# Performance work log

Hardware: AMD Instinct MI355X
Metric: run time of the kernel (lower is better)

Reference implementation:

```python
import jax, jax.numpy as jnp
import numpy as np

B, T, N, C = 32, 12, 2048, 1
D, K, H = 10, 2, 32


def setup_inputs() -> dict:
    key = jax.random.key(0)
    ks = jax.random.split(key, 8)
    s = 0.1  # small init scale for params
    return {
        "source": jax.random.normal(ks[0], (B, T, N, C), jnp.float32),
        "node_emb": jax.random.normal(ks[1], (N, D), jnp.float32),
        "gate_W": jax.random.normal(ks[2], (D, K, C + H, 2 * H), jnp.float32) * s,
        "gate_b": jax.random.normal(ks[3], (D, 2 * H), jnp.float32) * s,
        "upd_W": jax.random.normal(ks[4], (D, K, C + H, H), jnp.float32) * s,
        "upd_b": jax.random.normal(ks[5], (D, H), jnp.float32) * s,
        "conv_W": jax.random.normal(ks[6], (T * C, 1, 1, H), jnp.float32) * s,
        "conv_b": jax.random.normal(ks[7], (T * C,), jnp.float32) * s,
    }


def reference(source, node_emb, gate_W, gate_b, upd_W, upd_b, conv_W, conv_b):
    b, t, n, c = source.shape
    h = upd_W.shape[-1]
    k = gate_W.shape[1]
    dt = source.dtype
    E = node_emb

    # Adaptive adjacency from node embeddings (time-invariant -> hoist out of scan)
    A = jax.nn.softmax(jax.nn.relu(E @ E.T), axis=1)  # [N,N]
    sup = [jnp.eye(n, dtype=dt), A]
    for i in range(2, k):
        sup.append(2.0 * (A @ sup[-1]) - sup[-2])  # Chebyshev recursion
    S = jnp.stack(sup, 0)  # [K,N,N]

    # Node-specific weights/biases from embedding pools (also time-invariant)
    Wg = jnp.einsum('nd,dkio->nkio', E, gate_W)
    bg = E @ gate_b
    Wu = jnp.einsum('nd,dkio->nkio', E, upd_W)
    bu = E @ upd_b

    def gconv(x, W, bias):  # x: [B,N,Cin] -> [B,N,Cout]
        xg = jnp.einsum('knm,bmc->bnkc', S, x)
        return jnp.einsum('bnki,nkio->bno', xg, W) + bias

    def step(state, xt):  # GRU-style AGCRN cell
        xs = jnp.concatenate([xt, state], axis=-1)
        zr = jax.nn.sigmoid(gconv(xs, Wg, bg))
        z, r = jnp.split(zr, 2, axis=-1)
        hc = jnp.tanh(gconv(jnp.concatenate([xt, z * state], axis=-1), Wu, bu))
        hnew = r * state + (1.0 - r) * hc
        return hnew, None

    h0 = jnp.zeros((b, n, h), dtype=dt)
    h_last, _ = jax.lax.scan(step, h0, jnp.swapaxes(source, 0, 1))  # carry = last state

    # end_conv: Conv2d(1, T*C, kernel=(1,H)) on [B,1,N,H] == matmul over H
    out = jnp.einsum('bnh,oh->bon', h_last, conv_W[:, 0, 0, :]) + conv_b[None, :, None]
    out = out.reshape(b, t, c, n).transpose(0, 2, 3, 1)  # [B, C, N, T]
    return out
```

## Files before the change

### kernel.cpp

```cpp
#include <hip/hip_runtime.h>
#include <hip/hip_bf16.h>
#include <math.h>


#define NNODE 2048
#define NB 32
#define NT 12
#define NH 32
#define ND 10
#define NCOL 1024
#define NCX 384
#define KPAD 96
#define GPAD 104
#define WPAD 98

#define ASCALE 256.0f
#define AINV 0.00390625f

#define KSPLIT 4
#define KCHUNK 512
#define Y1S ((size_t)NNODE * NCOL)
#define AXPS ((size_t)NNODE * NCX)

typedef _Float16 half8 __attribute__((ext_vector_type(8)));
typedef float floatx4 __attribute__((ext_vector_type(4)));

#define AS1 __attribute__((address_space(1)))
#define AS3 __attribute__((address_space(3)))
__device__ __forceinline__ void gload16(const _Float16* g, _Float16* l) {
    __builtin_amdgcn_global_load_lds((const AS1 unsigned int*)(g),
                                     (AS3 unsigned int*)(l), 16, 0, 0);
}

constexpr size_t OFF_AH  = 0;
constexpr size_t OFF_WGT = OFF_AH + 2097152u;
constexpr size_t OFF_WUT = OFF_WGT + 6291456u;
constexpr size_t OFF_BG  = OFF_WUT + 3145728u;
constexpr size_t OFF_BU  = OFF_BG + 131072u;
constexpr size_t OFF_XT  = OFF_BU + 65536u;
constexpr size_t OFF_X2T = OFF_XT + 1048576u;
constexpr size_t OFF_SXT = OFF_X2T + 1048576u;
constexpr size_t OFF_HS  = OFF_SXT + 393216u;
constexpr size_t OFF_Y   = OFF_HS + 2097152u;
constexpr size_t OFF_AXP = OFF_Y + 4194304u;
constexpr size_t OFF_R   = OFF_AXP + 1572864u;
constexpr size_t OFF_ZH  = OFF_R + 1048576u;

__global__ __launch_bounds__(256) void adj_kernel(const float* __restrict__ E,
                                                  _Float16* __restrict__ Ah) {
    __shared__ float En[ND];
    __shared__ float red[256];
    const int n = blockIdx.x;
    const int t = threadIdx.x;
    if (t < ND) En[t] = E[n * ND + t];
    __syncthreads();
    float v[8];
    float mx = 0.f;
#pragma unroll
    for (int i = 0; i < 8; ++i) {
        const int m = t + i * 256;
        float acc = 0.f;
#pragma unroll
        for (int d = 0; d < ND; ++d) acc += En[d] * E[m * ND + d];
        acc = fmaxf(acc, 0.f);
        v[i] = acc;
        mx = fmaxf(mx, acc);
    }
    red[t] = mx;
    __syncthreads();
    for (int s = 128; s > 0; s >>= 1) {
        if (t < s) red[t] = fmaxf(red[t], red[t + s]);
        __syncthreads();
    }
    mx = red[0];
    __syncthreads();
    float sum = 0.f;
#pragma unroll
    for (int i = 0; i < 8; ++i) {
        v[i] = expf(v[i] - mx);
        sum += v[i];
    }
    red[t] = sum;
    __syncthreads();
    for (int s = 128; s > 0; s >>= 1) {
        if (t < s) red[t] += red[t + s];
        __syncthreads();
    }
    const float inv = ASCALE / red[0];
#pragma unroll
    for (int i = 0; i < 8; ++i)
        Ah[(size_t)n * NNODE + t + i * 256] = (_Float16)(v[i] * inv);
}

__global__ __launch_bounds__(256) void wg_kernel(const float* __restrict__ E,
                                                 const float* __restrict__ gW,
                                                 _Float16* __restrict__ Wgt) {
    __shared__ float Es[ND];
    __shared__ _Float16 Wl[64 * WPAD];
    const int n = blockIdx.x, t = threadIdx.x;
    if (t < ND) Es[t] = E[n * ND + t];
    for (int i = t; i < 64 * WPAD / 2; i += 256) ((unsigned*)Wl)[i] = 0u;
    __syncthreads();
    for (int rem = t; rem < 4224; rem += 256) {
        float acc = 0.f;
#pragma unroll
        for (int d = 0; d < ND; ++d) acc += Es[d] * gW[d * 4224 + rem];
        const int kk = rem / 2112, r2 = rem % 2112;
        const int i = r2 >> 6, o = r2 & 63;
        Wl[o * WPAD + kk * 33 + i] = (_Float16)acc;
    }
    __syncthreads();
    const unsigned* wl = (const unsigned*)Wl;
    unsigned* dst = (unsigned*)(Wgt + (size_t)n * 6144);
    for (int idx = t; idx < 64 * 48; idx += 256) {
        const int o = idx / 48, j = idx % 48;
        dst[idx] = wl[o * (WPAD / 2) + j];
    }
}

__global__ __launch_bounds__(256) void wu_kernel(const float* __restrict__ E,
                                                 const float* __restrict__ uW,
                                                 _Float16* __restrict__ Wut) {
    __shared__ float Es[ND];
    __shared__ _Float16 Wl[32 * WPAD];
    const int n = blockIdx.x, t = threadIdx.x;
    if (t < ND) Es[t] = E[n * ND + t];
    for (int i = t; i < 32 * WPAD / 2; i += 256) ((unsigned*)Wl)[i] = 0u;
    __syncthreads();
    for (int rem = t; rem < 2112; rem += 256) {
        float acc = 0.f;
#pragma unroll
        for (int d = 0; d < ND; ++d) acc += Es[d] * uW[d * 2112 + rem];
        const int kk = rem / 1056, r2 = rem % 1056;
        const int i = r2 >> 5, o = r2 & 31;
        Wl[o * WPAD + kk * 33 + i] = (_Float16)acc;
    }
    __syncthreads();
    const unsigned* wl = (const unsigned*)Wl;
    unsigned* dst = (unsigned*)(Wut + (size_t)n * 3072);
    for (int idx = t; idx < 32 * 48; idx += 256) {
        const int o = idx / 48, j = idx % 48;
        dst[idx] = wl[o * (WPAD / 2) + j];
    }
}

__global__ __launch_bounds__(256) void bias_kernel(const float* __restrict__ E,
                                                   const float* __restrict__ gb,
                                                   const float* __restrict__ ub,
                                                   float* __restrict__ bg,
                                                   float* __restrict__ bu) {
    const int idx = blockIdx.x * 256 + threadIdx.x;
    if (idx < NNODE * 64) {
        const int n = idx >> 6, o = idx & 63;
        float acc = 0.f;
#pragma unroll
        for (int d = 0; d < ND; ++d) acc += E[n * ND + d] * gb[d * 64 + o];
        bg[idx] = acc;
    } else if (idx < NNODE * 64 + NNODE * 32) {
        const int j = idx - NNODE * 64;
        const int n = j >> 5, o = j & 31;
        float acc = 0.f;
#pragma unroll
        for (int d = 0; d < ND; ++d) acc += E[n * ND + d] * ub[d * 32 + o];
        bu[j] = acc;
    }
}

__global__ __launch_bounds__(256) void setup_kernel(const float* __restrict__ src,
                                                    _Float16* __restrict__ XT,
                                                    _Float16* __restrict__ X2T,
                                                    _Float16* __restrict__ SXT,
                                                    float* __restrict__ Hs) {
    const int idx = blockIdx.x * 256 + threadIdx.x;
    XT[idx] = (_Float16)0.f;
    X2T[idx] = (_Float16)0.f;
    Hs[idx] = 0.f;
    if (idx < NCX * NNODE) {
        const int col = idx / NNODE, n = idx % NNODE;
        const int tt = col >> 5, b = col & 31;
        SXT[idx] = (_Float16)src[((size_t)b * NT + tt) * NNODE + n];
    }
}

__global__ __launch_bounds__(256) void mm_kernel(const _Float16* __restrict__ Ah,
                                                 const _Float16* __restrict__ XT,
                                                 _Float16* __restrict__ Y, int nct) {
    __shared__ _Float16 As[128 * 32];
    __shared__ _Float16 Bs[128 * 32];
    const int t = threadIdx.x;
    const int bid = blockIdx.x;
    const int xcd = bid & 7;
    const int kz = xcd >> 1;
    const int s = (bid >> 3) * 2 + (xcd & 1);
    const int m0 = (s & 15) * 128;
    const int c0 = (s >> 4) * 128;
    const int ncols = nct << 7;
    _Float16* __restrict__ Yp = Y + (size_t)kz * NNODE * ncols;
    const int lane = t & 63;
    const int w = t >> 6;
    const int wm = (w & 1) * 64;
    const int wn = (w >> 1) * 64;
    const int lm = lane & 15;
    const int q = lane >> 4;

    const int srow = w * 32 + (lane >> 2);
    const int sq = (lane & 3) ^ ((lane >> 3) & 3);
    const _Float16* gA = Ah + (size_t)(m0 + srow) * NNODE + kz * KCHUNK + sq * 8;
    const _Float16* gB = XT + (size_t)(c0 + srow) * NNODE + kz * KCHUNK + sq * 8;
    _Float16* lA = As + w * 1024;
    _Float16* lB = Bs + w * 1024;

    const int fp = (q ^ ((lm >> 1) & 3)) * 8;

    floatx4 acc[4][4] = {};

    for (int kt = 0; kt < KCHUNK; kt += 32) {
        gload16(gA, lA);
        gload16(gA + 16 * NNODE, lA + 512);
        gload16(gB, lB);
        gload16(gB + 16 * NNODE, lB + 512);
        gA += 32;
        gB += 32;
        __syncthreads();
        half8 af[4], bf[4];
#pragma unroll
        for (int mt = 0; mt < 4; ++mt)
            af[mt] = *(const half8*)&As[(wm + mt * 16 + lm) * 32 + fp];
#pragma unroll
        for (int nt = 0; nt < 4; ++nt)
            bf[nt] = *(const half8*)&Bs[(wn + nt * 16 + lm) * 32 + fp];
#pragma unroll
        for (int mt = 0; mt < 4; ++mt)
#pragma unroll
            for (int nt = 0; nt < 4; ++nt)
                acc[mt][nt] = __builtin_amdgcn_mfma_f32_16x16x32_f16(
                    af[mt], bf[nt], acc[mt][nt], 0, 0, 0);
        __syncthreads();
    }
#pragma unroll
    for (int mt = 0; mt < 4; ++mt) {
#pragma unroll
        for (int nt = 0; nt < 4; ++nt) {
            const int row = m0 + wm + mt * 16 + q * 4;
            const int col = c0 + wn + nt * 16 + lm;
#pragma unroll
            for (int r = 0; r < 4; ++r)
                Yp[(size_t)(row + r) * ncols + col] = (_Float16)(acc[mt][nt][r] * AINV);
        }
    }
}

__global__ __launch_bounds__(256) void gate_kernel(const float* __restrict__ src, int tcur,
                                                   const _Float16* __restrict__ Y,
                                                   const _Float16* __restrict__ AXP,
                                                   const _Float16* __restrict__ Wgt,
                                                   const float* __restrict__ bg,
                                                   const float* __restrict__ Hs,
                                                   _Float16* __restrict__ X2T,
                                                   _Float16* __restrict__ zh,
                                                   _Float16* __restrict__ rbuf) {
    __shared__ _Float16 catL[4][32][GPAD];
    const int t = threadIdx.x;
    const int n0 = blockIdx.x * 4;
    {
        const int pair = t >> 1, which = t & 1;
        const int nd = pair >> 5, b = pair & 31;
        const int n1 = n0 + nd;
        if (which == 0) {
            catL[nd][b][0] = (_Float16)src[((size_t)b * NT + tcur) * NNODE + n1];
            const float* hp = Hs + (size_t)n1 * 1024 + b * 32;
#pragma unroll
            for (int i = 0; i < 32; ++i) catL[nd][b][1 + i] = (_Float16)hp[i];
#pragma unroll
            for (int i = 66; i < KPAD; i += 2) *(unsigned*)&catL[nd][b][i] = 0u;
        } else {
            const _Float16* ax = AXP + (size_t)n1 * NCX + tcur * 32 + b;
            catL[nd][b][33] = (_Float16)((float)ax[0] + (float)ax[AXPS] +
                                         (float)ax[2 * AXPS] + (float)ax[3 * AXPS]);
            const _Float16* yp = Y + (size_t)n1 * NCOL + b * 32;
#pragma unroll
            for (int i = 0; i < 32; ++i) {
                const float sv = (float)yp[i] + (float)yp[Y1S + i] +
                                 (float)yp[2 * Y1S + i] + (float)yp[3 * Y1S + i];
                catL[nd][b][34 + i] = (_Float16)sv;
            }
        }
    }
    __syncthreads();
    const int w = t >> 6, lane = t & 63, lm = lane & 15, q = lane >> 4;
    const int n = n0 + w;
    const _Float16* Wn = Wgt + (size_t)n * 6144;
    floatx4 acc[2][4] = {};
#pragma unroll
    for (int kt = 0; kt < 3; ++kt) {
        half8 af[2], bf[4];
#pragma unroll
        for (int mt = 0; mt < 2; ++mt)
            af[mt] = *(const half8*)&catL[w][mt * 16 + lm][kt * 32 + q * 8];
#pragma unroll
        for (int nt = 0; nt < 4; ++nt)
            bf[nt] = *(const half8*)(Wn + (nt * 16 + lm) * KPAD + kt * 32 + q * 8);
#pragma unroll
        for (int mt = 0; mt < 2; ++mt)
#pragma unroll
            for (int nt = 0; nt < 4; ++nt)
                acc[mt][nt] = __builtin_amdgcn_mfma_f32_16x16x32_f16(
                    af[mt], bf[nt], acc[mt][nt], 0, 0, 0);
    }
#pragma unroll
    for (int nt = 0; nt < 4; ++nt) {
        const int o = nt * 16 + lm;
        const float bias = bg[n * 64 + o];
#pragma unroll
        for (int mt = 0; mt < 2; ++mt) {
#pragma unroll
            for (int r = 0; r < 4; ++r) {
                const int b = mt * 16 + q * 4 + r;
                const float s = 1.f / (1.f + expf(-(acc[mt][nt][r] + bias)));
                if (o < 32) {
                    const float hold = Hs[(size_t)n * 1024 + b * 32 + o];
                    const _Float16 zv = (_Float16)(s * hold);
                    zh[(size_t)n * 1024 + b * 32 + o] = zv;
                    X2T[(size_t)(b * 32 + o) * NNODE + n] = zv;
                } else {
                    rbuf[(size_t)n * 1024 + b * 32 + (o - 32)] = (_Float16)s;
                }
            }
        }
    }
}

__global__ __launch_bounds__(256) void upd_kernel(const float* __restrict__ src, int tcur,
                                                  const _Float16* __restrict__ Y,
                                                  const _Float16* __restrict__ AXP,
                                                  const _Float16* __restrict__ Wut,
                                                  const float* __restrict__ bu,
                                                  const _Float16* __restrict__ zh,
                                                  const _Float16* __restrict__ rbuf,
                                                  float* __restrict__ Hs,
                                                  _Float16* __restrict__ XT) {
    __shared__ _Float16 catL[4][32][GPAD];
    const int t = threadIdx.x;
    const int n0 = blockIdx.x * 4;
    {
        const int pair = t >> 1, which = t & 1;
        const int nd = pair >> 5, b = pair & 31;
        const int n1 = n0 + nd;
        if (which == 0) {
            catL[nd][b][0] = (_Float16)src[((size_t)b * NT + tcur) * NNODE + n1];
            const _Float16* zp = zh + (size_t)n1 * 1024 + b * 32;
#pragma unroll
            for (int i = 0; i < 32; ++i) catL[nd][b][1 + i] = zp[i];
#pragma unroll
            for (int i = 66; i < KPAD; i += 2) *(unsigned*)&catL[nd][b][i] = 0u;
        } else {
            const _Float16* ax = AXP + (size_t)n1 * NCX + tcur * 32 + b;
            catL[nd][b][33] = (_Float16)((float)ax[0] + (float)ax[AXPS] +
                                         (float)ax[2 * AXPS] + (float)ax[3 * AXPS]);
            const _Float16* yp = Y + (size_t)n1 * NCOL + b * 32;
#pragma unroll
            for (int i = 0; i < 32; ++i) {
                const float sv = (float)yp[i] + (float)yp[Y1S + i] +
                                 (float)yp[2 * Y1S + i] + (float)yp[3 * Y1S + i];
                catL[nd][b][34 + i] = (_Float16)sv;
            }
        }
    }
    __syncthreads();
    const int w = t >> 6, lane = t & 63, lm = lane & 15, q = lane >> 4;
    const int n = n0 + w;
    const _Float16* Wn = Wut + (size_t)n * 3072;
    floatx4 acc[2][2] = {};
#pragma unroll
    for (int kt = 0; kt < 3; ++kt) {
        half8 af[2], bf[2];
#pragma unroll
        for (int mt = 0; mt < 2; ++mt)
            af[mt] = *(const half8*)&catL[w][mt * 16 + lm][kt * 32 + q * 8];
#pragma unroll
        for (int nt = 0; nt < 2; ++nt)
            bf[nt] = *(const half8*)(Wn + (nt * 16 + lm) * KPAD + kt * 32 + q * 8);
#pragma unroll
        for (int mt = 0; mt < 2; ++mt)
#pragma unroll
            for (int nt = 0; nt < 2; ++nt)
                acc[mt][nt] = __builtin_amdgcn_mfma_f32_16x16x32_f16(
                    af[mt], bf[nt], acc[mt][nt], 0, 0, 0);
    }
#pragma unroll
    for (int nt = 0; nt < 2; ++nt) {
        const int o = nt * 16 + lm;
        const float bias = bu[n * 32 + o];
#pragma unroll
        for (int mt = 0; mt < 2; ++mt) {
#pragma unroll
            for (int r = 0; r < 4; ++r) {
                const int b = mt * 16 + q * 4 + r;
                const float hc = tanhf(acc[mt][nt][r] + bias);
                const float rr = (float)rbuf[(size_t)n * 1024 + b * 32 + o];
                const size_t hidx = (size_t)n * 1024 + b * 32 + o;
                const float hnew = rr * Hs[hidx] + (1.f - rr) * hc;
                Hs[hidx] = hnew;
                XT[(size_t)(b * 32 + o) * NNODE + n] = (_Float16)hnew;
            }
        }
    }
}

__global__ __launch_bounds__(256) void out_kernel(const float* __restrict__ Hs,
                                                  const float* __restrict__ cw,
                                                  const float* __restrict__ cb,
                                                  float* __restrict__ out) {
    __shared__ float h[NB * NH];
    __shared__ float cws[NT * NH];
    __shared__ float cbs[NT];
    const int n = blockIdx.x;
    const int t = threadIdx.x;
    for (int i = t; i < NT * NH; i += 256) cws[i] = cw[i];
    if (t < NT) cbs[t] = cb[t];
    for (int i = t; i < NB * NH; i += 256) h[i] = Hs[(size_t)n * 1024 + i];
    __syncthreads();
    for (int p = t; p < NB * NT; p += 256) {
        const int b = p / NT, tt = p % NT;
        float acc = cbs[tt];
#pragma unroll
        for (int j = 0; j < NH; ++j) acc += h[b * NH + j] * cws[tt * NH + j];
        out[(size_t)b * NNODE * NT + (size_t)n * NT + tt] = acc;
    }
}

extern "C" void kernel_launch(void* const* d_in, const int* in_sizes, int n_in,
                              void* d_out, int out_size, void* d_ws, size_t ws_size,
                              hipStream_t stream) {
    const float* src  = (const float*)d_in[0];
    const float* E    = (const float*)d_in[1];
    const float* gW   = (const float*)d_in[2];
    const float* gb   = (const float*)d_in[3];
    const float* uW   = (const float*)d_in[4];
    const float* ub   = (const float*)d_in[5];
    const float* cw   = (const float*)d_in[6];
    const float* cb   = (const float*)d_in[7];
    float* out = (float*)d_out;

    float* ws = (float*)d_ws;
    _Float16* Ah  = (_Float16*)(ws + OFF_AH);
    _Float16* Wgt = (_Float16*)(ws + OFF_WGT);
    _Float16* Wut = (_Float16*)(ws + OFF_WUT);
    float* bg  = ws + OFF_BG;
    float* bu  = ws + OFF_BU;
    _Float16* XT  = (_Float16*)(ws + OFF_XT);
    _Float16* X2T = (_Float16*)(ws + OFF_X2T);
    _Float16* SXT = (_Float16*)(ws + OFF_SXT);
    float* Hs  = ws + OFF_HS;
    _Float16* Y   = (_Float16*)(ws + OFF_Y);
    _Float16* AXP = (_Float16*)(ws + OFF_AXP);
    _Float16* rb  = (_Float16*)(ws + OFF_R);
    _Float16* zh  = (_Float16*)(ws + OFF_ZH);

    adj_kernel<<<NNODE, 256, 0, stream>>>(E, Ah);
    wg_kernel<<<NNODE, 256, 0, stream>>>(E, gW, Wgt);
    wu_kernel<<<NNODE, 256, 0, stream>>>(E, uW, Wut);
    bias_kernel<<<(NNODE * 96 + 255) / 256, 256, 0, stream>>>(E, gb, ub, bg, bu);
    setup_kernel<<<NNODE * NCOL / 256, 256, 0, stream>>>(src, XT, X2T, SXT, Hs);

    mm_kernel<<<64 * 3, 256, 0, stream>>>(Ah, SXT, AXP, 3);

    for (int t = 0; t < NT; ++t) {
        mm_kernel<<<64 * 8, 256, 0, stream>>>(Ah, XT, Y, 8);
        gate_kernel<<<NNODE / 4, 256, 0, stream>>>(src, t, Y, AXP, Wgt, bg, Hs, X2T, zh, rb);
        mm_kernel<<<64 * 8, 256, 0, stream>>>(Ah, X2T, Y, 8);
        upd_kernel<<<NNODE / 4, 256, 0, stream>>>(src, t, Y, AXP, Wut, bu, zh, rb, Hs, XT);
    }
    out_kernel<<<NNODE, 256, 0, stream>>>(Hs, cw, cb, out);
}
```

Before: 1.167 ms.

## Fuse recurrent loop into persistent megakernel with software grid barriers

Replaces the 48 per-step launches (matmul, gate, matmul, update) plus the setup and output kernels with one persistent kernel. Phases are separated by an atomic-counter grid barrier. This removes launch overhead and the gaps between kernels, and shares LDS between the matmul tiles and the gate/update staging. It relies on every block being co-resident; if occupancy is misjudged the barrier can deadlock. Serialized barriers and fewer blocks than before (256/512) may also reduce parallelism in some phases.

```diff
diff --git a/kernel.cpp b/kernel.cpp
--- a/kernel.cpp
+++ b/kernel.cpp
@@ -1,7 +1,6 @@
 #include <hip/hip_runtime.h>
 #include <hip/hip_bf16.h>
 #include <math.h>
-
 
 #define NNODE 2048
 #define NB 32
@@ -17,7 +16,6 @@
 #define ASCALE 256.0f
 #define AINV 0.00390625f
 
-#define KSPLIT 4
 #define KCHUNK 512
 #define Y1S ((size_t)NNODE * NCOL)
 #define AXPS ((size_t)NNODE * NCX)
@@ -45,6 +43,28 @@
 constexpr size_t OFF_AXP = OFF_Y + 4194304u;
 constexpr size_t OFF_R   = OFF_AXP + 1572864u;
 constexpr size_t OFF_ZH  = OFF_R + 1048576u;
+constexpr size_t OFF_BAR = OFF_ZH + 1048576u;
+
+__device__ __forceinline__ void gbar(unsigned* bar, int nb) {
+    __syncthreads();
+    if (threadIdx.x == 0) {
+        unsigned g = __hip_atomic_load(bar + 1, __ATOMIC_RELAXED, __HIP_MEMORY_SCOPE_AGENT);
+        unsigned a = __hip_atomic_fetch_add(bar, 1u, __ATOMIC_ACQ_REL, __HIP_MEMORY_SCOPE_AGENT);
+        if (a == (unsigned)nb - 1u) {
+            __hip_atomic_store(bar, 0u, __ATOMIC_RELAXED, __HIP_MEMORY_SCOPE_AGENT);
+            __hip_atomic_store(bar + 1, g + 1u, __ATOMIC_RELEASE, __HIP_MEMORY_SCOPE_AGENT);
+        } else {
+            while (__hip_atomic_load(bar + 1, __ATOMIC_ACQUIRE, __HIP_MEMORY_SCOPE_AGENT) == g)
+                __builtin_amdgcn_s_sleep(2);
+        }
+    }
+    __syncthreads();
+}
+
+__global__ void bar_init(unsigned* bar) {
+    __hip_atomic_store(bar, 0u, __ATOMIC_RELEASE, __HIP_MEMORY_SCOPE_AGENT);
+    __hip_atomic_store(bar + 1, 0u, __ATOMIC_RELEASE, __HIP_MEMORY_SCOPE_AGENT);
+}
 
 __global__ __launch_bounds__(256) void adj_kernel(const float* __restrict__ E,
                                                   _Float16* __restrict__ Ah) {
@@ -166,32 +186,13 @@
     }
 }
 
-__global__ __launch_bounds__(256) void setup_kernel(const float* __restrict__ src,
-                                                    _Float16* __restrict__ XT,
-                                                    _Float16* __restrict__ X2T,
-                                                    _Float16* __restrict__ SXT,
-                                                    float* __restrict__ Hs) {
-    const int idx = blockIdx.x * 256 + threadIdx.x;
-    XT[idx] = (_Float16)0.f;
-    X2T[idx] = (_Float16)0.f;
-    Hs[idx] = 0.f;
-    if (idx < NCX * NNODE) {
-        const int col = idx / NNODE, n = idx % NNODE;
-        const int tt = col >> 5, b = col & 31;
-        SXT[idx] = (_Float16)src[((size_t)b * NT + tt) * NNODE + n];
-    }
-}
-
-__global__ __launch_bounds__(256) void mm_kernel(const _Float16* __restrict__ Ah,
-                                                 const _Float16* __restrict__ XT,
-                                                 _Float16* __restrict__ Y, int nct) {
-    __shared__ _Float16 As[128 * 32];
-    __shared__ _Float16 Bs[128 * 32];
-    const int t = threadIdx.x;
-    const int bid = blockIdx.x;
-    const int xcd = bid & 7;
+__device__ __forceinline__ void mm_tile(const _Float16* __restrict__ Ah,
+                                        const _Float16* __restrict__ XT,
+                                        _Float16* __restrict__ Y, int nct,
+                                        int task, int t, _Float16* As, _Float16* Bs) {
+    const int xcd = task & 7;
     const int kz = xcd >> 1;
-    const int s = (bid >> 3) * 2 + (xcd & 1);
+    const int s = (task >> 3) * 2 + (xcd & 1);
     const int m0 = (s & 15) * 128;
     const int c0 = (s >> 4) * 128;
     const int ncols = nct << 7;
@@ -209,7 +210,6 @@
     const _Float16* gB = XT + (size_t)(c0 + srow) * NNODE + kz * KCHUNK + sq * 8;
     _Float16* lA = As + w * 1024;
     _Float16* lB = Bs + w * 1024;
-
     const int fp = (q ^ ((lm >> 1) & 3)) * 8;
 
     floatx4 acc[4][4] = {};
@@ -250,181 +250,199 @@
     }
 }
 
-__global__ __launch_bounds__(256) void gate_kernel(const float* __restrict__ src, int tcur,
-                                                   const _Float16* __restrict__ Y,
-                                                   const _Float16* __restrict__ AXP,
-                                                   const _Float16* __restrict__ Wgt,
-                                                   const float* __restrict__ bg,
-                                                   const float* __restrict__ Hs,
-                                                   _Float16* __restrict__ X2T,
-                                                   _Float16* __restrict__ zh,
-                                                   _Float16* __restrict__ rbuf) {
-    __shared__ _Float16 catL[4][32][GPAD];
+#define CAT(nd, b, i) cat[((nd) * 32 + (b)) * GPAD + (i)]
+
+__global__ __launch_bounds__(256, 2) void mega_kernel(
+    const float* __restrict__ src, const _Float16* __restrict__ Ah,
+    const _Float16* __restrict__ Wgt, const _Float16* __restrict__ Wut,
+    const float* __restrict__ bg, const float* __restrict__ bu,
+    const float* __restrict__ cw, const float* __restrict__ cb,
+    _Float16* __restrict__ XT, _Float16* __restrict__ X2T,
+    _Float16* __restrict__ SXT, float* __restrict__ Hs,
+    _Float16* __restrict__ Y, _Float16* __restrict__ AXP,
+    _Float16* __restrict__ rbuf, _Float16* __restrict__ zh,
+    float* __restrict__ out, unsigned* bar, int nb) {
+    __shared__ __align__(16) _Float16 smem[4 * 32 * GPAD];
+    _Float16* As = smem;
+    _Float16* Bs = smem + 4096;
+    _Float16* cat = smem;
     const int t = threadIdx.x;
-    const int n0 = blockIdx.x * 4;
+    const int bid = blockIdx.x;
+    const int w = t >> 6, lane = t & 63, lm = lane & 15, q = lane >> 4;
+
     {
-        const int pair = t >> 1, which = t & 1;
-        const int nd = pair >> 5, b = pair & 31;
-        const int n1 = n0 + nd;
-        if (which == 0) {
-            catL[nd][b][0] = (_Float16)src[((size_t)b * NT + tcur) * NNODE + n1];
-            const float* hp = Hs + (size_t)n1 * 1024 + b * 32;
-#pragma unroll
-            for (int i = 0; i < 32; ++i) catL[nd][b][1 + i] = (_Float16)hp[i];
-#pragma unroll
-            for (int i = 66; i < KPAD; i += 2) *(unsigned*)&catL[nd][b][i] = 0u;
-        } else {
-            const _Float16* ax = AXP + (size_t)n1 * NCX + tcur * 32 + b;
-            catL[nd][b][33] = (_Float16)((float)ax[0] + (float)ax[AXPS] +
-                                         (float)ax[2 * AXPS] + (float)ax[3 * AXPS]);
-            const _Float16* yp = Y + (size_t)n1 * NCOL + b * 32;
-#pragma unroll
-            for (int i = 0; i < 32; ++i) {
-                const float sv = (float)yp[i] + (float)yp[Y1S + i] +
-                                 (float)yp[2 * Y1S + i] + (float)yp[3 * Y1S + i];
-                catL[nd][b][34 + i] = (_Float16)sv;
-            }
+        unsigned* p = (unsigned*)XT;
+        for (int idx = bid * 256 + t; idx < 1048576; idx += nb * 256) p[idx] = 0u;
+        unsigned* ph = (unsigned*)Hs;
+        for (int idx = bid * 256 + t; idx < 2097152; idx += nb * 256) ph[idx] = 0u;
+        for (int idx = bid * 256 + t; idx < NCX * NNODE; idx += nb * 256) {
+            const int col = idx >> 11, n = idx & 2047;
+            const int tt = col >> 5, b = col & 31;
+            SXT[idx] = (_Float16)src[((size_t)b * NT + tt) * NNODE + n];
         }
     }
-    __syncthreads();
-    const int w = t >> 6, lane = t & 63, lm = lane & 15, q = lane >> 4;
-    const int n = n0 + w;
-    const _Float16* Wn = Wgt + (size_t)n * 6144;
-    floatx4 acc[2][4] = {};
-#pragma unroll
-    for (int kt = 0; kt < 3; ++kt) {
-        half8 af[2], bf[4];
-#pragma unroll
-        for (int mt = 0; mt < 2; ++mt)
-            af[mt] = *(const half8*)&catL[w][mt * 16 + lm][kt * 32 + q * 8];
-#pragma unroll
-        for (int nt = 0; nt < 4; ++nt)
-            bf[nt] = *(const half8*)(Wn + (nt * 16 + lm) * KPAD + kt * 32 + q * 8);
-#pragma unroll
-        for (int mt = 0; mt < 2; ++mt)
-#pragma unroll
-            for (int nt = 0; nt < 4; ++nt)
-                acc[mt][nt] = __builtin_amdgcn_mfma_f32_16x16x32_f16(
-                    af[mt], bf[nt], acc[mt][nt], 0, 0, 0);
-    }
-#pragma unroll
-    for (int nt = 0; nt < 4; ++nt) {
-        const int o = nt * 16 + lm;
-        const float bias = bg[n * 64 + o];
-#pragma unroll
-        for (int mt = 0; mt < 2; ++mt) {
-#pragma unroll
-            for (int r = 0; r < 4; ++r) {
-                const int b = mt * 16 + q * 4 + r;
-                const float s = 1.f / (1.f + expf(-(acc[mt][nt][r] + bias)));
-                if (o < 32) {
-                    const float hold = Hs[(size_t)n * 1024 + b * 32 + o];
-                    const _Float16 zv = (_Float16)(s * hold);
-                    zh[(size_t)n * 1024 + b * 32 + o] = zv;
-                    X2T[(size_t)(b * 32 + o) * NNODE + n] = zv;
+    gbar(bar, nb);
+
+    for (int task = bid; task < 192; task += nb)
+        mm_tile(Ah, SXT, AXP, 3, task, t, As, Bs);
+    gbar(bar, nb);
+
+    for (int step = 0; step < NT; ++step) {
+        for (int task = bid; task < 512; task += nb)
+            mm_tile(Ah, XT, Y, 8, task, t, As, Bs);
+        gbar(bar, nb);
+
+        for (int g = bid; g < 512; g += nb) {
+            const int n0 = g * 4;
+            {
+                const int pair = t >> 1, which = t & 1;
+                const int nd = pair >> 5, b = pair & 31;
+                const int n1 = n0 + nd;
+                if (which == 0) {
+                    CAT(nd, b, 0) = (_Float16)src[((size_t)b * NT + step) * NNODE + n1];
+                    const float* hp = Hs + (size_t)n1 * 1024 + b * 32;
+#pragma unroll
+                    for (int i = 0; i < 32; ++i) CAT(nd, b, 1 + i) = (_Float16)hp[i];
+#pragma unroll
+                    for (int i = 66; i < KPAD; i += 2) *(unsigned*)&CAT(nd, b, i) = 0u;
                 } else {
-                    rbuf[(size_t)n * 1024 + b * 32 + (o - 32)] = (_Float16)s;
+                    const _Float16* ax = AXP + (size_t)n1 * NCX + step * 32 + b;
+                    CAT(nd, b, 33) = (_Float16)((float)ax[0] + (float)ax[AXPS] +
+                                                (float)ax[2 * AXPS] + (float)ax[3 * AXPS]);
+                    const _Float16* yp = Y + (size_t)n1 * NCOL + b * 32;
+#pragma unroll
+                    for (int i = 0; i < 32; ++i) {
+                        const float sv = (float)yp[i] + (float)yp[Y1S + i] +
+                                         (float)yp[2 * Y1S + i] + (float)yp[3 * Y1S + i];
+                        CAT(nd, b, 34 + i) = (_Float16)sv;
+                    }
                 }
             }
+            __syncthreads();
+            const int n = n0 + w;
+            const _Float16* Wn = Wgt + (size_t)n * 6144;
+            floatx4 acc[2][4] = {};
+#pragma unroll
+            for (int kt = 0; kt < 3; ++kt) {
+                half8 af[2], bf[4];
+#pragma unroll
+                for (int mt = 0; mt < 2; ++mt)
+                    af[mt] = *(const half8*)&CAT(w, mt * 16 + lm, kt * 32 + q * 8);
+#pragma unroll
+                for (int nt = 0; nt < 4; ++nt)
+                    bf[nt] = *(const half8*)(Wn + (nt * 16 + lm) * KPAD + kt * 32 + q * 8);
+#pragma unroll
+                for (int mt = 0; mt < 2; ++mt)
+#pragma unroll
+                    for (int nt = 0; nt < 4; ++nt)
+                        acc[mt][nt] = __builtin_amdgcn_mfma_f32_16x16x32_f16(
+                            af[mt], bf[nt], acc[mt][nt], 0, 0, 0);
+            }
+#pragma unroll
+            for (int nt = 0; nt < 4; ++nt) {
+                const int o = nt * 16 + lm;
+                const float bias = bg[n * 64 + o];
+#pragma unroll
+                for (int mt = 0; mt < 2; ++mt) {
+#pragma unroll
+                    for (int r = 0; r < 4; ++r) {
+                        const int b = mt * 16 + q * 4 + r;
+                        const float s = 1.f / (1.f + expf(-(acc[mt][nt][r] + bias)));
+                        if (o < 32) {
+                            const float hold = Hs[(size_t)n * 1024 + b * 32 + o];
+                            const _Float16 zv = (_Float16)(s * hold);
+                            zh[(size_t)n * 1024 + b * 32 + o] = zv;
+                            X2T[(size_t)(b * 32 + o) * NNODE + n] = zv;
+                        } else {
+                            rbuf[(size_t)n * 1024 + b * 32 + (o - 32)] = (_Float16)s;
+                        }
+                    }
+                }
+            }
+            __syncthreads();
         }
-    }
-}
-
-__global__ __launch_bounds__(256) void upd_kernel(const float* __restrict__ src, int tcur,
-                                                  const _Float16* __restrict__ Y,
-                                                  const _Float16* __restrict__ AXP,
-                                                  const _Float16* __restrict__ Wut,
-                                                  const float* __restrict__ bu,
-                                                  const _Float16* __restrict__ zh,
-                                                  const _Float16* __restrict__ rbuf,
-                                                  float* __restrict__ Hs,
-                                                  _Float16* __restrict__ XT) {
-    __shared__ _Float16 catL[4][32][GPAD];
-    const int t = threadIdx.x;
-    const int n0 = blockIdx.x * 4;
-    {
-        const int pair = t >> 1, which = t & 1;
-        const int nd = pair >> 5, b = pair & 31;
-        const int n1 = n0 + nd;
-        if (which == 0) {
-            catL[nd][b][0] = (_Float16)src[((size_t)b * NT + tcur) * NNODE + n1];
-            const _Float16* zp = zh + (size_t)n1 * 1024 + b * 32;
-#pragma unroll
-            for (int i = 0; i < 32; ++i) catL[nd][b][1 + i] = zp[i];
-#pragma unroll
-            for (int i = 66; i < KPAD; i += 2) *(unsigned*)&catL[nd][b][i] = 0u;
-        } else {
-            const _Float16* ax = AXP + (size_t)n1 * NCX + tcur * 32 + b;
-            catL[nd][b][33] = (_Float16)((float)ax[0] + (float)ax[AXPS] +
-                                         (float)ax[2 * AXPS] + (float)ax[3 * AXPS]);
-            const _Float16* yp = Y + (size_t)n1 * NCOL + b * 32;
-#pragma unroll
-            for (int i = 0; i < 32; ++i) {
-                const float sv = (float)yp[i] + (float)yp[Y1S + i] +
-                                 (float)yp[2 * Y1S + i] + (float)yp[3 * Y1S + i];
-                catL[nd][b][34 + i] = (_Float16)sv;
-            }
+        gbar(bar, nb);
+
+        for (int task = bid; task < 512; task += nb)
+            mm_tile(Ah, X2T, Y, 8, task, t, As, Bs);
+        gbar(bar, nb);
+
+        for (int g = bid; g < 512; g += nb) {
+            const int n0 = g * 4;
+            {
+                const int pair = t >> 1, which = t & 1;
+                const int nd = pair >> 5, b = pair & 31;
+                const int n1 = n0 + nd;
+                if (which == 0) {
+                    CAT(nd, b, 0) = (_Float16)src[((size_t)b * NT + step) * NNODE + n1];
+                    const _Float16* zp = zh + (size_t)n1 * 1024 + b * 32;
+#pragma unroll
+                    for (int i = 0; i < 32; ++i) CAT(nd, b, 1 + i) = zp[i];
+#pragma unroll
+                    for (int i = 66; i < KPAD; i += 2) *(unsigned*)&CAT(nd, b, i) = 0u;
+                } else {
+                    const _Float16* ax = AXP + (size_t)n1 * NCX + step * 32 + b;
+                    CAT(nd, b, 33) = (_Float16)((float)ax[0] + (float)ax[AXPS] +
+                                                (float)ax[2 * AXPS] + (float)ax[3 * AXPS]);
+                    const _Float16* yp = Y + (size_t)n1 * NCOL + b * 32;
+#pragma unroll
+                    for (int i = 0; i < 32; ++i) {
+                        const float sv = (float)yp[i] + (float)yp[Y1S + i] +
+                                         (float)yp[2 * Y1S + i] + (float)yp[3 * Y1S + i];
+                        CAT(nd, b, 34 + i) = (_Float16)sv;
+                    }
+                }
+            }
+            __syncthreads();
+            const int n = n0 + w;
+            const _Float16* Wn = Wut + (size_t)n * 3072;
+            floatx4 acc[2][2] = {};
+#pragma unroll
+            for (int kt = 0; kt < 3; ++kt) {
+                half8 af[2], bf[2];
+#pragma unroll
+                for (int mt = 0; mt < 2; ++mt)
+                    af[mt] = *(const half8*)&CAT(w, mt * 16 + lm, kt * 32 + q * 8);
+#pragma unroll
+                for (int nt = 0; nt < 2; ++nt)
+                    bf[nt] = *(const half8*)(Wn + (nt * 16 + lm) * KPAD + kt * 32 + q * 8);
+#pragma unroll
+                for (int mt = 0; mt < 2; ++mt)
+#pragma unroll
+                    for (int nt = 0; nt < 2; ++nt)
+                        acc[mt][nt] = __builtin_amdgcn_mfma_f32_16x16x32_f16(
+                            af[mt], bf[nt], acc[mt][nt], 0, 0, 0);
+            }
+#pragma unroll
+            for (int nt = 0; nt < 2; ++nt) {
+                const int o = nt * 16 + lm;
+                const float bias = bu[n * 32 + o];
+#pragma unroll
+                for (int mt = 0; mt < 2; ++mt) {
+#pragma unroll
+                    for (int r = 0; r < 4; ++r) {
+                        const int b = mt * 16 + q * 4 + r;
+                        const float hc = tanhf(acc[mt][nt][r] + bias);
+                        const float rr = (float)rbuf[(size_t)n * 1024 + b * 32 + o];
+                        const size_t hidx = (size_t)n * 1024 + b * 32 + o;
+                        const float hnew = rr * Hs[hidx] + (1.f - rr) * hc;
+                        Hs[hidx] = hnew;
+                        XT[(size_t)(b * 32 + o) * NNODE + n] = (_Float16)hnew;
+                    }
+                }
+            }
+            __syncthreads();
         }
-    }
-    __syncthreads();
-    const int w = t >> 6, lane = t & 63, lm = lane & 15, q = lane >> 4;
-    const int n = n0 + w;
-    const _Float16* Wn = Wut + (size_t)n * 3072;
-    floatx4 acc[2][2] = {};
-#pragma unroll
-    for (int kt = 0; kt < 3; ++kt) {
-        half8 af[2], bf[2];
-#pragma unroll
-        for (int mt = 0; mt < 2; ++mt)
-            af[mt] = *(const half8*)&catL[w][mt * 16 + lm][kt * 32 + q * 8];
-#pragma unroll
-        for (int nt = 0; nt < 2; ++nt)
-            bf[nt] = *(const half8*)(Wn + (nt * 16 + lm) * KPAD + kt * 32 + q * 8);
-#pragma unroll
-        for (int mt = 0; mt < 2; ++mt)
-#pragma unroll
-            for (int nt = 0; nt < 2; ++nt)
-                acc[mt][nt] = __builtin_amdgcn_mfma_f32_16x16x32_f16(
-                    af[mt], bf[nt], acc[mt][nt], 0, 0, 0);
-    }
-#pragma unroll
-    for (int nt = 0; nt < 2; ++nt) {
-        const int o = nt * 16 + lm;
-        const float bias = bu[n * 32 + o];
-#pragma unroll
-        for (int mt = 0; mt < 2; ++mt) {
-#pragma unroll
-            for (int r = 0; r < 4; ++r) {
-                const int b = mt * 16 + q * 4 + r;
-                const float hc = tanhf(acc[mt][nt][r] + bias);
-                const float rr = (float)rbuf[(size_t)n * 1024 + b * 32 + o];
-                const size_t hidx = (size_t)n * 1024 + b * 32 + o;
-                const float hnew = rr * Hs[hidx] + (1.f - rr) * hc;
-                Hs[hidx] = hnew;
-                XT[(size_t)(b * 32 + o) * NNODE + n] = (_Float16)hnew;
-            }
-        }
-    }
-}
-
-__global__ __launch_bounds__(256) void out_kernel(const float* __restrict__ Hs,
-                                                  const float* __restrict__ cw,
-                                                  const float* __restrict__ cb,
-                                                  float* __restrict__ out) {
-    __shared__ float h[NB * NH];
-    __shared__ float cws[NT * NH];
-    __shared__ float cbs[NT];
-    const int n = blockIdx.x;
-    const int t = threadIdx.x;
-    for (int i = t; i < NT * NH; i += 256) cws[i] = cw[i];
-    if (t < NT) cbs[t] = cb[t];
-    for (int i = t; i < NB * NH; i += 256) h[i] = Hs[(size_t)n * 1024 + i];
-    __syncthreads();
-    for (int p = t; p < NB * NT; p += 256) {
-        const int b = p / NT, tt = p % NT;
-        float acc = cbs[tt];
-#pragma unroll
-        for (int j = 0; j < NH; ++j) acc += h[b * NH + j] * cws[tt * NH + j];
+        gbar(bar, nb);
+    }
+
+    for (int p = bid * 256 + t; p < NNODE * NB * NT; p += nb * 256) {
+        const int n = p / 384, rem = p % 384;
+        const int b = rem / NT, tt = rem % NT;
+        float acc = cb[tt];
+        const float* hp = Hs + (size_t)n * 1024 + b * 32;
+#pragma unroll
+        for (int j = 0; j < NH; ++j) acc += hp[j] * cw[tt * 32 + j];
         out[(size_t)b * NNODE * NT + (size_t)n * NT + tt] = acc;
     }
 }
@@ -456,20 +474,19 @@
     _Float16* AXP = (_Float16*)(ws + OFF_AXP);
     _Float16* rb  = (_Float16*)(ws + OFF_R);
     _Float16* zh  = (_Float16*)(ws + OFF_ZH);
+    unsigned* bar = (unsigned*)(ws + OFF_BAR);
 
     adj_kernel<<<NNODE, 256, 0, stream>>>(E, Ah);
     wg_kernel<<<NNODE, 256, 0, stream>>>(E, gW, Wgt);
     wu_kernel<<<NNODE, 256, 0, stream>>>(E, uW, Wut);
     bias_kernel<<<(NNODE * 96 + 255) / 256, 256, 0, stream>>>(E, gb, ub, bg, bu);
-    setup_kernel<<<NNODE * NCOL / 256, 256, 0, stream>>>(src, XT, X2T, SXT, Hs);
-
-    mm_kernel<<<64 * 3, 256, 0, stream>>>(Ah, SXT, AXP, 3);
-
-    for (int t = 0; t < NT; ++t) {
-        mm_kernel<<<64 * 8, 256, 0, stream>>>(Ah, XT, Y, 8);
-        gate_kernel<<<NNODE / 4, 256, 0, stream>>>(src, t, Y, AXP, Wgt, bg, Hs, X2T, zh, rb);
-        mm_kernel<<<64 * 8, 256, 0, stream>>>(Ah, X2T, Y, 8);
-        upd_kernel<<<NNODE / 4, 256, 0, stream>>>(src, t, Y, AXP, Wut, bu, zh, rb, Hs, XT);
-    }
-    out_kernel<<<NNODE, 256, 0, stream>>>(Hs, cw, cb, out);
-}
+    bar_init<<<1, 1, 0, stream>>>(bar);
+
+    int occ = 0;
+    hipOccupancyMaxActiveBlocksPerMultiprocessor(&occ, mega_kernel, 256, 0);
+    const int nb = (occ >= 2) ? 512 : 256;
+
+    mega_kernel<<<nb, 256, 0, stream>>>(src, Ah, Wgt, Wut, bg, bu, cw, cb,
+                                        XT, X2T, SXT, Hs, Y, AXP, rb, zh,
+                                        out, bar, nb);
+}
```

Result: slower. 3.411 ms (+192.4%).

## Fuse propagation matmul with gate/update cells using per-row-chunk atomic counters

Applied to the files above, without the earlier changes.

Each step's mm_kernel is merged into the gate and update kernels, giving one 512-block kernel per half-step. Each block first computes one matmul tile and signals an atomic counter for its row chunk. It then spin-waits until all 32 tiles covering its node rows are done before running the GRU cell. This removes half the per-step launches and the full-grid barriers between matmul and cell, and shares LDS between the two phases. It relies on all 512 blocks being co-resident (two per CU under the launch bounds) to avoid deadlock, and it adds spin-wait and fence overhead.

```diff
diff --git a/kernel.cpp b/kernel.cpp
--- a/kernel.cpp
+++ b/kernel.cpp
@@ -1,7 +1,6 @@
 #include <hip/hip_runtime.h>
 #include <hip/hip_bf16.h>
 #include <math.h>
-
 
 #define NNODE 2048
 #define NB 32
@@ -17,7 +16,6 @@
 #define ASCALE 256.0f
 #define AINV 0.00390625f
 
-#define KSPLIT 4
 #define KCHUNK 512
 #define Y1S ((size_t)NNODE * NCOL)
 #define AXPS ((size_t)NNODE * NCX)
@@ -45,6 +43,7 @@
 constexpr size_t OFF_AXP = OFF_Y + 4194304u;
 constexpr size_t OFF_R   = OFF_AXP + 1572864u;
 constexpr size_t OFF_ZH  = OFF_R + 1048576u;
+constexpr size_t OFF_CNT = OFF_ZH + 1048576u;
 
 __global__ __launch_bounds__(256) void adj_kernel(const float* __restrict__ E,
                                                   _Float16* __restrict__ Ah) {
@@ -170,28 +169,27 @@
                                                     _Float16* __restrict__ XT,
                                                     _Float16* __restrict__ X2T,
                                                     _Float16* __restrict__ SXT,
-                                                    float* __restrict__ Hs) {
+                                                    float* __restrict__ Hs,
+                                                    unsigned* __restrict__ cnt) {
     const int idx = blockIdx.x * 256 + threadIdx.x;
     XT[idx] = (_Float16)0.f;
     X2T[idx] = (_Float16)0.f;
     Hs[idx] = 0.f;
     if (idx < NCX * NNODE) {
-        const int col = idx / NNODE, n = idx % NNODE;
+        const int col = idx >> 11, n = idx & 2047;
         const int tt = col >> 5, b = col & 31;
         SXT[idx] = (_Float16)src[((size_t)b * NT + tt) * NNODE + n];
     }
-}
-
-__global__ __launch_bounds__(256) void mm_kernel(const _Float16* __restrict__ Ah,
-                                                 const _Float16* __restrict__ XT,
-                                                 _Float16* __restrict__ Y, int nct) {
-    __shared__ _Float16 As[128 * 32];
-    __shared__ _Float16 Bs[128 * 32];
-    const int t = threadIdx.x;
-    const int bid = blockIdx.x;
-    const int xcd = bid & 7;
+    if (idx < 384) cnt[idx] = 0u;
+}
+
+__device__ __forceinline__ void mm_tile(const _Float16* __restrict__ Ah,
+                                        const _Float16* __restrict__ XT,
+                                        _Float16* __restrict__ Y, int nct,
+                                        int task, int t, _Float16* As, _Float16* Bs) {
+    const int xcd = task & 7;
     const int kz = xcd >> 1;
-    const int s = (bid >> 3) * 2 + (xcd & 1);
+    const int s = (task >> 3) * 2 + (xcd & 1);
     const int m0 = (s & 15) * 128;
     const int c0 = (s >> 4) * 128;
     const int ncols = nct << 7;
@@ -209,7 +207,6 @@
     const _Float16* gB = XT + (size_t)(c0 + srow) * NNODE + kz * KCHUNK + sq * 8;
     _Float16* lA = As + w * 1024;
     _Float16* lB = Bs + w * 1024;
-
     const int fp = (q ^ ((lm >> 1) & 3)) * 8;
 
     floatx4 acc[4][4] = {};
@@ -250,44 +247,69 @@
     }
 }
 
-__global__ __launch_bounds__(256) void gate_kernel(const float* __restrict__ src, int tcur,
-                                                   const _Float16* __restrict__ Y,
-                                                   const _Float16* __restrict__ AXP,
-                                                   const _Float16* __restrict__ Wgt,
-                                                   const float* __restrict__ bg,
-                                                   const float* __restrict__ Hs,
-                                                   _Float16* __restrict__ X2T,
-                                                   _Float16* __restrict__ zh,
-                                                   _Float16* __restrict__ rbuf) {
-    __shared__ _Float16 catL[4][32][GPAD];
-    const int t = threadIdx.x;
-    const int n0 = blockIdx.x * 4;
+__device__ __forceinline__ void signal_wait(unsigned* cnt, int bid, int t) {
+    __threadfence();
+    __syncthreads();
+    if (t == 0) {
+        const int sp = (bid >> 3) * 2 + (bid & 1);
+        __hip_atomic_fetch_add(&cnt[sp & 15], 1u, __ATOMIC_RELEASE,
+                               __HIP_MEMORY_SCOPE_AGENT);
+        const int rc = bid >> 5;
+        unsigned v;
+        do {
+            v = __hip_atomic_load(&cnt[rc], __ATOMIC_RELAXED, __HIP_MEMORY_SCOPE_AGENT);
+            if (v < 32u) __builtin_amdgcn_s_sleep(1);
+        } while (v < 32u);
+        (void)__hip_atomic_load(&cnt[rc], __ATOMIC_ACQUIRE, __HIP_MEMORY_SCOPE_AGENT);
+    }
+    __syncthreads();
+}
+
+#define CAT(nd, b, i) cat[((nd) * 32 + (b)) * GPAD + (i)]
+
+__global__ __launch_bounds__(256, 2) void mmgate_kernel(
+    const float* __restrict__ src, int tcur, const _Float16* __restrict__ Ah,
+    const _Float16* __restrict__ XT, _Float16* __restrict__ Y,
+    const _Float16* __restrict__ AXP, const _Float16* __restrict__ Wgt,
+    const float* __restrict__ bg, const float* __restrict__ Hs,
+    _Float16* __restrict__ X2T, _Float16* __restrict__ zh,
+    _Float16* __restrict__ rbuf, unsigned* __restrict__ cnt) {
+    __shared__ __align__(16) _Float16 smem[4 * 32 * GPAD];
+    _Float16* As = smem;
+    _Float16* Bs = smem + 4096;
+    _Float16* cat = smem;
+    const int t = threadIdx.x, bid = blockIdx.x;
+    const int w = t >> 6, lane = t & 63, lm = lane & 15, q = lane >> 4;
+
+    mm_tile(Ah, XT, Y, 8, bid, t, As, Bs);
+    signal_wait(cnt, bid, t);
+
+    const int n0 = bid * 4;
     {
         const int pair = t >> 1, which = t & 1;
         const int nd = pair >> 5, b = pair & 31;
         const int n1 = n0 + nd;
         if (which == 0) {
-            catL[nd][b][0] = (_Float16)src[((size_t)b * NT + tcur) * NNODE + n1];
+            CAT(nd, b, 0) = (_Float16)src[((size_t)b * NT + tcur) * NNODE + n1];
             const float* hp = Hs + (size_t)n1 * 1024 + b * 32;
 #pragma unroll
-            for (int i = 0; i < 32; ++i) catL[nd][b][1 + i] = (_Float16)hp[i];
-#pragma unroll
-            for (int i = 66; i < KPAD; i += 2) *(unsigned*)&catL[nd][b][i] = 0u;
+            for (int i = 0; i < 32; ++i) CAT(nd, b, 1 + i) = (_Float16)hp[i];
+#pragma unroll
+            for (int i = 66; i < KPAD; i += 2) *(unsigned*)&CAT(nd, b, i) = 0u;
         } else {
             const _Float16* ax = AXP + (size_t)n1 * NCX + tcur * 32 + b;
-            catL[nd][b][33] = (_Float16)((float)ax[0] + (float)ax[AXPS] +
-                                         (float)ax[2 * AXPS] + (float)ax[3 * AXPS]);
+            CAT(nd, b, 33) = (_Float16)((float)ax[0] + (float)ax[AXPS] +
+                                        (float)ax[2 * AXPS] + (float)ax[3 * AXPS]);
             const _Float16* yp = Y + (size_t)n1 * NCOL + b * 32;
 #pragma unroll
             for (int i = 0; i < 32; ++i) {
                 const float sv = (float)yp[i] + (float)yp[Y1S + i] +
                                  (float)yp[2 * Y1S + i] + (float)yp[3 * Y1S + i];
-                catL[nd][b][34 + i] = (_Float16)sv;
+                CAT(nd, b, 34 + i) = (_Float16)sv;
             }
         }
     }
     __syncthreads();
-    const int w = t >> 6, lane = t & 63, lm = lane & 15, q = lane >> 4;
     const int n = n0 + w;
     const _Float16* Wn = Wgt + (size_t)n * 6144;
     floatx4 acc[2][4] = {};
@@ -296,7 +318,7 @@
         half8 af[2], bf[4];
 #pragma unroll
         for (int mt = 0; mt < 2; ++mt)
-            af[mt] = *(const half8*)&catL[w][mt * 16 + lm][kt * 32 + q * 8];
+            af[mt] = *(const half8*)&CAT(w, mt * 16 + lm, kt * 32 + q * 8);
 #pragma unroll
         for (int nt = 0; nt < 4; ++nt)
             bf[nt] = *(const half8*)(Wn + (nt * 16 + lm) * KPAD + kt * 32 + q * 8);
@@ -330,44 +352,49 @@
     }
 }
 
-__global__ __launch_bounds__(256) void upd_kernel(const float* __restrict__ src, int tcur,
-                                                  const _Float16* __restrict__ Y,
-                                                  const _Float16* __restrict__ AXP,
-                                                  const _Float16* __restrict__ Wut,
-                                                  const float* __restrict__ bu,
-                                                  const _Float16* __restrict__ zh,
-                                                  const _Float16* __restrict__ rbuf,
-                                                  float* __restrict__ Hs,
-                                                  _Float16* __restrict__ XT) {
-    __shared__ _Float16 catL[4][32][GPAD];
-    const int t = threadIdx.x;
-    const int n0 = blockIdx.x * 4;
+__global__ __launch_bounds__(256, 2) void mmupd_kernel(
+    const float* __restrict__ src, int tcur, const _Float16* __restrict__ Ah,
+    const _Float16* __restrict__ X2T, _Float16* __restrict__ Y,
+    const _Float16* __restrict__ AXP, const _Float16* __restrict__ Wut,
+    const float* __restrict__ bu, const _Float16* __restrict__ zh,
+    const _Float16* __restrict__ rbuf, float* __restrict__ Hs,
+    _Float16* __restrict__ XT, unsigned* __restrict__ cnt) {
+    __shared__ __align__(16) _Float16 smem[4 * 32 * GPAD];
+    _Float16* As = smem;
+    _Float16* Bs = smem + 4096;
+    _Float16* cat = smem;
+    const int t = threadIdx.x, bid = blockIdx.x;
+    const int w = t >> 6, lane = t & 63, lm = lane & 15, q = lane >> 4;
+
+    mm_tile(Ah, X2T, Y, 8, bid, t, As, Bs);
+    signal_wait(cnt, bid, t);
+
+    const int n0 = bid * 4;
     {
         const int pair = t >> 1, which = t & 1;
         const int nd = pair >> 5, b = pair & 31;
         const int n1 = n0 + nd;
         if (which == 0) {
-            catL[nd][b][0] = (_Float16)src[((size_t)b * NT + tcur) * NNODE + n1];
+            CAT(nd, b, 0) = (_Float16)src[((size_t)b * NT + tcur) * NNODE + n1];
             const _Float16* zp = zh + (size_t)n1 * 1024 + b * 32;
 #pragma unroll
-            for (int i = 0; i < 32; ++i) catL[nd][b][1 + i] = zp[i];
-#pragma unroll
-            for (int i = 66; i < KPAD; i += 2) *(unsigned*)&catL[nd][b][i] = 0u;
+            for (int i = 0; i < 32; ++i) CAT(nd, b, 1 + i) = zp[i];
+#pragma unroll
+            for (int i = 66; i < KPAD; i += 2) *(unsigned*)&CAT(nd, b, i) = 0u;
         } else {
             const _Float16* ax = AXP + (size_t)n1 * NCX + tcur * 32 + b;
-            catL[nd][b][33] = (_Float16)((float)ax[0] + (float)ax[AXPS] +
-                                         (float)ax[2 * AXPS] + (float)ax[3 * AXPS]);
+            CAT(nd, b, 33) = (_Float16)((float)ax[0] + (float)ax[AXPS] +
+                                        (float)ax[2 * AXPS] + (float)ax[3 * AXPS]);
             const _Float16* yp = Y + (size_t)n1 * NCOL + b * 32;
 #pragma unroll
             for (int i = 0; i < 32; ++i) {
                 const float sv = (float)yp[i] + (float)yp[Y1S + i] +
                                  (float)yp[2 * Y1S + i] + (float)yp[3 * Y1S + i];
-                catL[nd][b][34 + i] = (_Float16)sv;
+                CAT(nd, b, 34 + i) = (_Float16)sv;
             }
         }
     }
     __syncthreads();
-    const int w = t >> 6, lane = t & 63, lm = lane & 15, q = lane >> 4;
     const int n = n0 + w;
     const _Float16* Wn = Wut + (size_t)n * 3072;
     floatx4 acc[2][2] = {};
@@ -376,7 +403,7 @@
         half8 af[2], bf[2];
 #pragma unroll
         for (int mt = 0; mt < 2; ++mt)
-            af[mt] = *(const half8*)&catL[w][mt * 16 + lm][kt * 32 + q * 8];
+            af[mt] = *(const half8*)&CAT(w, mt * 16 + lm, kt * 32 + q * 8);
 #pragma unroll
         for (int nt = 0; nt < 2; ++nt)
             bf[nt] = *(const half8*)(Wn + (nt * 16 + lm) * KPAD + kt * 32 + q * 8);
@@ -405,6 +432,13 @@
             }
         }
     }
+}
+
+__global__ __launch_bounds__(256) void mm_kernel(const _Float16* __restrict__ Ah,
+                                                 const _Float16* __restrict__ XT,
+                                                 _Float16* __restrict__ Y, int nct) {
+    __shared__ __align__(16) _Float16 smem[8192];
+    mm_tile(Ah, XT, Y, nct, blockIdx.x, threadIdx.x, smem, smem + 4096);
 }
 
 __global__ __launch_bounds__(256) void out_kernel(const float* __restrict__ Hs,
@@ -456,20 +490,21 @@
     _Float16* AXP = (_Float16*)(ws + OFF_AXP);
     _Float16* rb  = (_Float16*)(ws + OFF_R);
     _Float16* zh  = (_Float16*)(ws + OFF_ZH);
+    unsigned* cnt = (unsigned*)(ws + OFF_CNT);
 
     adj_kernel<<<NNODE, 256, 0, stream>>>(E, Ah);
     wg_kernel<<<NNODE, 256, 0, stream>>>(E, gW, Wgt);
     wu_kernel<<<NNODE, 256, 0, stream>>>(E, uW, Wut);
     bias_kernel<<<(NNODE * 96 + 255) / 256, 256, 0, stream>>>(E, gb, ub, bg, bu);
-    setup_kernel<<<NNODE * NCOL / 256, 256, 0, stream>>>(src, XT, X2T, SXT, Hs);
+    setup_kernel<<<NNODE * NCOL / 256, 256, 0, stream>>>(src, XT, X2T, SXT, Hs, cnt);
 
     mm_kernel<<<64 * 3, 256, 0, stream>>>(Ah, SXT, AXP, 3);
 
     for (int t = 0; t < NT; ++t) {
-        mm_kernel<<<64 * 8, 256, 0, stream>>>(Ah, XT, Y, 8);
-        gate_kernel<<<NNODE / 4, 256, 0, stream>>>(src, t, Y, AXP, Wgt, bg, Hs, X2T, zh, rb);
-        mm_kernel<<<64 * 8, 256, 0, stream>>>(Ah, X2T, Y, 8);
-        upd_kernel<<<NNODE / 4, 256, 0, stream>>>(src, t, Y, AXP, Wut, bu, zh, rb, Hs, XT);
+        mmgate_kernel<<<512, 256, 0, stream>>>(src, t, Ah, XT, Y, AXP, Wgt, bg,
+                                               Hs, X2T, zh, rb, cnt + 32 * t);
+        mmupd_kernel<<<512, 256, 0, stream>>>(src, t, Ah, X2T, Y, AXP, Wut, bu,
+                                              zh, rb, Hs, XT, cnt + 32 * t + 16);
     }
     out_kernel<<<NNODE, 256, 0, stream>>>(Hs, cw, cb, out);
 }
```

Measured after the change: 3.559 ms. +205.0%, slower.
